# Kernel optimization log

Hardware: AMD Instinct MI355X
Metric: run time of the kernel (lower is better)

Reference implementation:

```python
import jax, jax.numpy as jnp
import numpy as np

NEG_INF = -1e30
LRELU_SLOPE = 0.01
KEEP_SCALE = 2.0  # 1/(1-p) with p=0.5


def mixed_act(x, tid):
    # x: [B, H], tid: [H] int type ids
    # 0 relu, 1 tanh, 2 sig, 3 'smin'->Softmax, 4 'smax'->Softmin, 5 gelu, 6 lrelu
    relu = jnp.maximum(x, 0.0)
    tanh = jnp.tanh(x)
    sig = jax.nn.sigmoid(x)
    gelu = jax.nn.gelu(x, approximate=False)
    lrelu = jnp.where(x >= 0, x, LRELU_SLOPE * x)
    # softmax/softmin restricted to the columns of that type (matches x[:, idx] gather)
    smin = jax.nn.softmax(jnp.where(tid == 3, x, NEG_INF), axis=1)
    smax = jax.nn.softmax(jnp.where(tid == 4, -x, NEG_INF), axis=1)
    return jnp.select(
        [tid == 0, tid == 1, tid == 2, tid == 3, tid == 4, tid == 5, tid == 6],
        [relu, tanh, sig, smin, smax, gelu, lrelu],
    )


def setup_inputs() -> dict:
    key = jax.random.key(0)
    ks = jax.random.split(key, 16)
    B, D_IN, H, C = 32768, 784, 1024, 10
    s_in, s_h = 1.0 / np.sqrt(D_IN), 1.0 / np.sqrt(H)
    inp = {
        "x": jax.random.normal(ks[0], (B, D_IN), jnp.float32),
        "W0": jax.random.normal(ks[1], (H, D_IN), jnp.float32) * s_in,
        "b0": jax.random.normal(ks[2], (H,), jnp.float32) * s_in,
        "W1": jax.random.normal(ks[3], (H, H), jnp.float32) * s_h,
        "b1": jax.random.normal(ks[4], (H,), jnp.float32) * s_h,
        "W2": jax.random.normal(ks[5], (H, H), jnp.float32) * s_h,
        "b2": jax.random.normal(ks[6], (H,), jnp.float32) * s_h,
        "W3": jax.random.normal(ks[7], (C, H), jnp.float32) * s_h,
        "b3": jax.random.normal(ks[8], (C,), jnp.float32) * s_h,
        "mask1": jax.random.bernoulli(ks[9], 0.5, (B, H)).astype(jnp.float32),
        "mask2": jax.random.bernoulli(ks[10], 0.5, (B, H)).astype(jnp.float32),
        "mask3": jax.random.bernoulli(ks[11], 0.5, (B, H)).astype(jnp.float32),
        "type_ids": jax.random.randint(ks[12], (3, H), 0, 7, jnp.int32),
    }
    return inp


def reference(x, W0, b0, W1, b1, W2, b2, W3, b3, mask1, mask2, mask3, type_ids):
    h = mixed_act(x @ W0.T + b0, type_ids[0])
    h = mixed_act((h * mask1 * KEEP_SCALE) @ W1.T + b1, type_ids[1])
    h = mixed_act((h * mask2 * KEEP_SCALE) @ W2.T + b2, type_ids[2])
    logits = (h * mask3 * KEEP_SCALE) @ W3.T + b3
    out = jax.nn.log_softmax(logits, axis=1)
    return (out, mask1, mask2, mask3)
```

## Files before the change

kernel.cpp:

```cpp
#include <hip/hip_runtime.h>
#include <hip/hip_bf16.h>
#include <cstdint>
#include <cstddef>

typedef __bf16 bf16_t;
typedef bf16_t bf16x8 __attribute__((ext_vector_type(8)));
typedef bf16_t bf16x4 __attribute__((ext_vector_type(4)));
typedef float f32x4 __attribute__((ext_vector_type(4)));

#define NEG_BIG (-1e30f)

__global__ __launch_bounds__(256) void convert_pad(const float* __restrict__ src,
                                                   bf16_t* __restrict__ dst,
                                                   int incols, int outcols) {
    const int row = blockIdx.x;
    const float* s = src + (size_t)row * incols;
    bf16_t* d = dst + (size_t)row * outcols;
    const int n4 = outcols >> 2;
    for (int c = threadIdx.x; c < n4; c += blockDim.x) {
        const int col = c << 2;
        float4 v;
        if (col < incols) v = *(const float4*)(s + col);
        else              v = make_float4(0.f, 0.f, 0.f, 0.f);
        bf16x4 o;
        o[0] = (bf16_t)v.x; o[1] = (bf16_t)v.y; o[2] = (bf16_t)v.z; o[3] = (bf16_t)v.w;
        *(bf16x4*)(d + col) = o;
    }
}

#define BM 128
#define BN 128
#define BK 32

__global__ __launch_bounds__(256) void gemm_bt(const bf16_t* __restrict__ A,
                                               const bf16_t* __restrict__ W,
                                               const float* __restrict__ bias,
                                               bf16_t* __restrict__ Z,
                                               int K, int N) {
    __shared__ __align__(16) bf16_t As[BM * BK];
    __shared__ __align__(16) bf16_t Bs[BN * BK];
    const int tid  = threadIdx.x;
    const int wid  = tid >> 6;
    const int lane = tid & 63;
    const int n0 = blockIdx.x * BN;
    const int m0 = blockIdx.y * BM;

    const int wm = (wid >> 1) * 64;
    const int wn = (wid & 1) * 64;

    f32x4 acc[4][4] = {};

    const int srow0 = wid * 32 + (lane >> 2);
    const int scol  = (lane & 3) * 8;

    const bf16_t* Aptr0 = A + (size_t)(m0 + srow0) * K + scol;
    const bf16_t* Aptr1 = A + (size_t)(m0 + srow0 + 16) * K + scol;
    const bf16_t* Wptr0 = W + (size_t)(n0 + srow0) * K + scol;
    const bf16_t* Wptr1 = W + (size_t)(n0 + srow0 + 16) * K + scol;

    bf16_t* AsB0 = As + (wid * 2 + 0) * 512;
    bf16_t* AsB1 = As + (wid * 2 + 1) * 512;
    bf16_t* BsB0 = Bs + (wid * 2 + 0) * 512;
    bf16_t* BsB1 = Bs + (wid * 2 + 1) * 512;

    for (int k0 = 0; k0 < K; k0 += BK) {
        __syncthreads();
        __builtin_amdgcn_global_load_lds((const __attribute__((address_space(1))) void*)(Aptr0 + k0),
                                         (__attribute__((address_space(3))) void*)AsB0, 16, 0, 0);
        __builtin_amdgcn_global_load_lds((const __attribute__((address_space(1))) void*)(Aptr1 + k0),
                                         (__attribute__((address_space(3))) void*)AsB1, 16, 0, 0);
        __builtin_amdgcn_global_load_lds((const __attribute__((address_space(1))) void*)(Wptr0 + k0),
                                         (__attribute__((address_space(3))) void*)BsB0, 16, 0, 0);
        __builtin_amdgcn_global_load_lds((const __attribute__((address_space(1))) void*)(Wptr1 + k0),
                                         (__attribute__((address_space(3))) void*)BsB1, 16, 0, 0);
        __syncthreads();

        const int arow = wm + (lane & 15);
        const int brow = wn + (lane & 15);
        const int koff = (lane >> 4) * 8;
        bf16x8 af[4], bfr[4];
        #pragma unroll
        for (int i = 0; i < 4; ++i)
            af[i] = *(const bf16x8*)(As + (arow + i * 16) * BK + koff);
        #pragma unroll
        for (int j = 0; j < 4; ++j)
            bfr[j] = *(const bf16x8*)(Bs + (brow + j * 16) * BK + koff);
        #pragma unroll
        for (int i = 0; i < 4; ++i)
            #pragma unroll
            for (int j = 0; j < 4; ++j)
                acc[i][j] = __builtin_amdgcn_mfma_f32_16x16x32_bf16(af[i], bfr[j], acc[i][j], 0, 0, 0);
    }

    const int cq = lane >> 4;
    const int cl = lane & 15;
    #pragma unroll
    for (int j = 0; j < 4; ++j) {
        const int col = n0 + wn + j * 16 + cl;
        const float bj = bias[col];
        #pragma unroll
        for (int i = 0; i < 4; ++i) {
            const int row = m0 + wm + i * 16 + cq * 4;
            #pragma unroll
            for (int r = 0; r < 4; ++r)
                Z[(size_t)(row + r) * N + col] = (bf16_t)(acc[i][j][r] + bj);
        }
    }
}

__device__ __forceinline__ float wave_max(float v) {
    #pragma unroll
    for (int off = 32; off > 0; off >>= 1) v = fmaxf(v, __shfl_xor(v, off));
    return v;
}
__device__ __forceinline__ float wave_sum(float v) {
    #pragma unroll
    for (int off = 32; off > 0; off >>= 1) v += __shfl_xor(v, off);
    return v;
}

__global__ __launch_bounds__(256) void act_kernel(const bf16_t* __restrict__ Z,
                                                  const float* __restrict__ mask,
                                                  const int* __restrict__ tids,
                                                  bf16_t* __restrict__ H,
                                                  float* __restrict__ mask_out) {
    const int wid  = threadIdx.x >> 6;
    const int lane = threadIdx.x & 63;
    const int row  = blockIdx.x * 4 + wid;
    const size_t rb = (size_t)row * 1024;

    float z[16], mk[16];
    int   ty[16];
    #pragma unroll
    for (int c = 0; c < 4; ++c) {
        const int col = c * 256 + lane * 4;
        const bf16x4 zv = *(const bf16x4*)(Z + rb + col);
        const float4 mv = *(const float4*)(mask + rb + col);
        const int4   tv = *(const int4*)(tids + col);
        z[c*4+0] = (float)zv[0]; z[c*4+1] = (float)zv[1];
        z[c*4+2] = (float)zv[2]; z[c*4+3] = (float)zv[3];
        mk[c*4+0] = mv.x; mk[c*4+1] = mv.y; mk[c*4+2] = mv.z; mk[c*4+3] = mv.w;
        ty[c*4+0] = tv.x; ty[c*4+1] = tv.y; ty[c*4+2] = tv.z; ty[c*4+3] = tv.w;
    }

    float mx3 = NEG_BIG, mx4 = NEG_BIG;
    #pragma unroll
    for (int j = 0; j < 16; ++j) {
        if (ty[j] == 3) mx3 = fmaxf(mx3, z[j]);
        if (ty[j] == 4) mx4 = fmaxf(mx4, -z[j]);
    }
    mx3 = wave_max(mx3);
    mx4 = wave_max(mx4);

    float s3 = 0.f, s4 = 0.f;
    #pragma unroll
    for (int j = 0; j < 16; ++j) {
        if (ty[j] == 3) s3 += __expf(z[j] - mx3);
        if (ty[j] == 4) s4 += __expf(-z[j] - mx4);
    }
    s3 = wave_sum(s3);
    s4 = wave_sum(s4);
    const float inv3 = 1.f / s3;
    const float inv4 = 1.f / s4;

    #pragma unroll
    for (int c = 0; c < 4; ++c) {
        const int col = c * 256 + lane * 4;
        bf16x4 h4;
        float4 m4;
        #pragma unroll
        for (int j = 0; j < 4; ++j) {
            const int k = c * 4 + j;
            const float zz = z[k];
            const int   tt = ty[k];
            float a;
            if (tt == 0)      a = fmaxf(zz, 0.f);
            else if (tt == 1) { const float e = __expf(-2.f * fabsf(zz));
                                const float th = (1.f - e) / (1.f + e);
                                a = (zz >= 0.f) ? th : -th; }
            else if (tt == 2) a = 1.f / (1.f + __expf(-zz));
            else if (tt == 3) a = __expf(zz - mx3) * inv3;
            else if (tt == 4) a = __expf(-zz - mx4) * inv4;
            else if (tt == 5) a = 0.5f * zz * (1.f + erff(zz * 0.70710678118654752f));
            else              a = (zz >= 0.f) ? zz : 0.01f * zz;
            h4[j] = (bf16_t)(a * mk[k] * 2.0f);
        }
        m4.x = mk[c*4+0]; m4.y = mk[c*4+1]; m4.z = mk[c*4+2]; m4.w = mk[c*4+3];
        *(bf16x4*)(H + rb + col) = h4;
        *(float4*)(mask_out + rb + col) = m4;
    }
}

__global__ __launch_bounds__(256) void final_layer(const bf16_t* __restrict__ H,
                                                   const float* __restrict__ W3,
                                                   const float* __restrict__ b3,
                                                   float* __restrict__ out) {
    __shared__ __align__(16) bf16_t Ws[10 * 1024];
    for (int i = threadIdx.x; i < 10240; i += 256) Ws[i] = (bf16_t)W3[i];
    __syncthreads();
    const int wid  = threadIdx.x >> 6;
    const int lane = threadIdx.x & 63;
    #pragma unroll 1
    for (int rr = 0; rr < 4; ++rr) {
        const int row = blockIdx.x * 16 + wid * 4 + rr;
        const bf16_t* hrow = H + (size_t)row * 1024;
        float acc[10];
        #pragma unroll
        for (int n = 0; n < 10; ++n) acc[n] = 0.f;
        #pragma unroll
        for (int c = 0; c < 2; ++c) {
            const int k = c * 512 + lane * 8;
            const bf16x8 hv = *(const bf16x8*)(hrow + k);
            float hf[8];
            #pragma unroll
            for (int j = 0; j < 8; ++j) hf[j] = (float)hv[j];
            #pragma unroll
            for (int n = 0; n < 10; ++n) {
                const bf16x8 wv = *(const bf16x8*)(Ws + n * 1024 + k);
                #pragma unroll
                for (int j = 0; j < 8; ++j) acc[n] += hf[j] * (float)wv[j];
            }
        }
        #pragma unroll
        for (int n = 0; n < 10; ++n)
            #pragma unroll
            for (int off = 32; off > 0; off >>= 1)
                acc[n] += __shfl_down(acc[n], off);
        if (lane == 0) {
            float lg[10]; float mx = -1e30f;
            #pragma unroll
            for (int n = 0; n < 10; ++n) { lg[n] = acc[n] + b3[n]; mx = fmaxf(mx, lg[n]); }
            float se = 0.f;
            #pragma unroll
            for (int n = 0; n < 10; ++n) se += __expf(lg[n] - mx);
            const float lse = logf(se) + mx;
            #pragma unroll
            for (int n = 0; n < 10; ++n) out[(size_t)row * 10 + n] = lg[n] - lse;
        }
    }
}

extern "C" void kernel_launch(void* const* d_in, const int* in_sizes, int n_in,
                              void* d_out, int out_size, void* d_ws, size_t ws_size,
                              hipStream_t stream) {
    (void)in_sizes; (void)n_in; (void)out_size; (void)ws_size;
    const float* x     = (const float*)d_in[0];
    const float* W0    = (const float*)d_in[1];
    const float* b0    = (const float*)d_in[2];
    const float* W1    = (const float*)d_in[3];
    const float* b1    = (const float*)d_in[4];
    const float* W2    = (const float*)d_in[5];
    const float* b2    = (const float*)d_in[6];
    const float* W3    = (const float*)d_in[7];
    const float* b3    = (const float*)d_in[8];
    const float* mask1 = (const float*)d_in[9];
    const float* mask2 = (const float*)d_in[10];
    const float* mask3 = (const float*)d_in[11];
    const int*   tids  = (const int*)d_in[12];

    float* out = (float*)d_out;
    float* mo1 = out + 327680;
    float* mo2 = mo1 + 33554432;
    float* mo3 = mo2 + 33554432;

    char* ws = (char*)d_ws;
    bf16_t* xb  = (bf16_t*)ws;  ws += (size_t)32768 * 800 * 2;
    bf16_t* W0b = (bf16_t*)ws;  ws += (size_t)1024 * 800 * 2;
    bf16_t* W1b = (bf16_t*)ws;  ws += (size_t)1024 * 1024 * 2;
    bf16_t* W2b = (bf16_t*)ws;  ws += (size_t)1024 * 1024 * 2;
    bf16_t* Zb  = (bf16_t*)ws;  ws += (size_t)32768 * 1024 * 2;
    bf16_t* hb  = (bf16_t*)ws;  ws += (size_t)32768 * 1024 * 2;

    convert_pad<<<32768, 256, 0, stream>>>(x,  xb,  784, 800);
    convert_pad<<<1024,  256, 0, stream>>>(W0, W0b, 784, 800);
    convert_pad<<<1024,  256, 0, stream>>>(W1, W1b, 1024, 1024);
    convert_pad<<<1024,  256, 0, stream>>>(W2, W2b, 1024, 1024);

    dim3 g(1024 / BN, 32768 / BM);
    gemm_bt<<<g, 256, 0, stream>>>(xb, W0b, b0, Zb, 800, 1024);
    act_kernel<<<8192, 256, 0, stream>>>(Zb, mask1, tids, hb, mo1);
    gemm_bt<<<g, 256, 0, stream>>>(hb, W1b, b1, Zb, 1024, 1024);
    act_kernel<<<8192, 256, 0, stream>>>(Zb, mask2, tids + 1024, hb, mo2);
    gemm_bt<<<g, 256, 0, stream>>>(hb, W2b, b2, Zb, 1024, 1024);
    act_kernel<<<8192, 256, 0, stream>>>(Zb, mask3, tids + 2048, hb, mo3);
    final_layer<<<2048, 256, 0, stream>>>(hb, W3, b3, out);
}
```

Before: 1.199 ms.

## Fuse all forward stages into one persistent cooperative kernel with grid syncs

Replaces the eleven separate kernel launches with a single persistent cooperative kernel. Each stage is a grid-stride loop over its tiles or rows, and stages are separated by grid.sync(). This removes launch overhead and inter-kernel gaps. In exchange the grid is limited to the number of co-resident blocks, so the GEMM tiles lose some scheduling flexibility, and grid barriers add their own cost. The original multi-kernel path is kept as a fallback if the cooperative launch fails.

```diff
diff --git a/kernel.cpp b/kernel.cpp
--- a/kernel.cpp
+++ b/kernel.cpp
@@ -1,7 +1,10 @@
 #include <hip/hip_runtime.h>
 #include <hip/hip_bf16.h>
+#include <hip/hip_cooperative_groups.h>
 #include <cstdint>
 #include <cstddef>
+
+namespace cg = cooperative_groups;
 
 typedef __bf16 bf16_t;
 typedef bf16_t bf16x8 __attribute__((ext_vector_type(8)));
@@ -9,15 +12,18 @@
 typedef float f32x4 __attribute__((ext_vector_type(4)));
 
 #define NEG_BIG (-1e30f)
-
-__global__ __launch_bounds__(256) void convert_pad(const float* __restrict__ src,
-                                                   bf16_t* __restrict__ dst,
-                                                   int incols, int outcols) {
-    const int row = blockIdx.x;
+#define BM 128
+#define BN 128
+#define BK 32
+
+
+__device__ __forceinline__ void convert_row(const float* __restrict__ src,
+                                            bf16_t* __restrict__ dst,
+                                            int incols, int outcols, int row) {
     const float* s = src + (size_t)row * incols;
     bf16_t* d = dst + (size_t)row * outcols;
     const int n4 = outcols >> 2;
-    for (int c = threadIdx.x; c < n4; c += blockDim.x) {
+    for (int c = threadIdx.x; c < n4; c += 256) {
         const int col = c << 2;
         float4 v;
         if (col < incols) v = *(const float4*)(s + col);
@@ -28,22 +34,19 @@
     }
 }
 
-#define BM 128
-#define BN 128
-#define BK 32
-
-__global__ __launch_bounds__(256) void gemm_bt(const bf16_t* __restrict__ A,
-                                               const bf16_t* __restrict__ W,
-                                               const float* __restrict__ bias,
-                                               bf16_t* __restrict__ Z,
-                                               int K, int N) {
-    __shared__ __align__(16) bf16_t As[BM * BK];
-    __shared__ __align__(16) bf16_t Bs[BN * BK];
+__device__ __forceinline__ void gemm_tile(char* smem,
+                                          const bf16_t* __restrict__ A,
+                                          const bf16_t* __restrict__ W,
+                                          const float* __restrict__ bias,
+                                          bf16_t* __restrict__ Z,
+                                          int K, int tile) {
+    bf16_t* As = (bf16_t*)smem;
+    bf16_t* Bs = (bf16_t*)(smem + 8192);
     const int tid  = threadIdx.x;
     const int wid  = tid >> 6;
     const int lane = tid & 63;
-    const int n0 = blockIdx.x * BN;
-    const int m0 = blockIdx.y * BM;
+    const int n0 = (tile & 7) * BN;
+    const int m0 = (tile >> 3) * BM;
 
     const int wm = (wid >> 1) * 64;
     const int wn = (wid & 1) * 64;
@@ -103,7 +106,7 @@
             const int row = m0 + wm + i * 16 + cq * 4;
             #pragma unroll
             for (int r = 0; r < 4; ++r)
-                Z[(size_t)(row + r) * N + col] = (bf16_t)(acc[i][j][r] + bj);
+                Z[(size_t)(row + r) * 1024 + col] = (bf16_t)(acc[i][j][r] + bj);
         }
     }
 }
@@ -119,14 +122,14 @@
     return v;
 }
 
-__global__ __launch_bounds__(256) void act_kernel(const bf16_t* __restrict__ Z,
-                                                  const float* __restrict__ mask,
-                                                  const int* __restrict__ tids,
-                                                  bf16_t* __restrict__ H,
-                                                  float* __restrict__ mask_out) {
+__device__ __forceinline__ void act_rows(const bf16_t* __restrict__ Z,
+                                         const float* __restrict__ mask,
+                                         const int* __restrict__ tids,
+                                         bf16_t* __restrict__ H,
+                                         float* __restrict__ mask_out, int rg) {
     const int wid  = threadIdx.x >> 6;
     const int lane = threadIdx.x & 63;
-    const int row  = blockIdx.x * 4 + wid;
+    const int row  = rg * 4 + wid;
     const size_t rb = (size_t)row * 1024;
 
     float z[16], mk[16];
@@ -191,6 +194,115 @@
     }
 }
 
+__device__ __forceinline__ void final_block(const bf16_t* __restrict__ Ws,
+                                            const bf16_t* __restrict__ H,
+                                            const float* __restrict__ b3,
+                                            float* __restrict__ out, int b) {
+    const int wid  = threadIdx.x >> 6;
+    const int lane = threadIdx.x & 63;
+    #pragma unroll 1
+    for (int rr = 0; rr < 4; ++rr) {
+        const int row = b * 16 + wid * 4 + rr;
+        const bf16_t* hrow = H + (size_t)row * 1024;
+        float acc[10];
+        #pragma unroll
+        for (int n = 0; n < 10; ++n) acc[n] = 0.f;
+        #pragma unroll
+        for (int c = 0; c < 2; ++c) {
+            const int k = c * 512 + lane * 8;
+            const bf16x8 hv = *(const bf16x8*)(hrow + k);
+            float hf[8];
+            #pragma unroll
+            for (int j = 0; j < 8; ++j) hf[j] = (float)hv[j];
+            #pragma unroll
+            for (int n = 0; n < 10; ++n) {
+                const bf16x8 wv = *(const bf16x8*)(Ws + n * 1024 + k);
+                #pragma unroll
+                for (int j = 0; j < 8; ++j) acc[n] += hf[j] * (float)wv[j];
+            }
+        }
+        #pragma unroll
+        for (int n = 0; n < 10; ++n)
+            #pragma unroll
+            for (int off = 32; off > 0; off >>= 1)
+                acc[n] += __shfl_down(acc[n], off);
+        if (lane == 0) {
+            float lg[10]; float mx = -1e30f;
+            #pragma unroll
+            for (int n = 0; n < 10; ++n) { lg[n] = acc[n] + b3[n]; mx = fmaxf(mx, lg[n]); }
+            float se = 0.f;
+            #pragma unroll
+            for (int n = 0; n < 10; ++n) se += __expf(lg[n] - mx);
+            const float lse = logf(se) + mx;
+            #pragma unroll
+            for (int n = 0; n < 10; ++n) out[(size_t)row * 10 + n] = lg[n] - lse;
+        }
+    }
+}
+
+
+struct FusedParams {
+    const float *x, *W0, *b0, *W1, *b1, *W2, *b2, *W3, *b3;
+    const float *mask1, *mask2, *mask3;
+    const int* tids;
+    bf16_t *xb, *W0b, *W1b, *W2b, *Zb, *hb;
+    float *out, *mo1, *mo2, *mo3;
+};
+
+__global__ __launch_bounds__(256) void fused_forward(FusedParams p) {
+    cg::grid_group grid = cg::this_grid();
+    __shared__ __align__(16) char smem[20480];
+    const int nb  = gridDim.x;
+    const int bid = blockIdx.x;
+
+    for (int r = bid; r < 32768; r += nb) convert_row(p.x,  p.xb,  784, 800, r);
+    for (int r = bid; r < 1024;  r += nb) convert_row(p.W0, p.W0b, 784, 800, r);
+    for (int r = bid; r < 1024;  r += nb) convert_row(p.W1, p.W1b, 1024, 1024, r);
+    for (int r = bid; r < 1024;  r += nb) convert_row(p.W2, p.W2b, 1024, 1024, r);
+    grid.sync();
+    for (int t = bid; t < 2048; t += nb) gemm_tile(smem, p.xb, p.W0b, p.b0, p.Zb, 800, t);
+    grid.sync();
+    for (int r = bid; r < 8192; r += nb) act_rows(p.Zb, p.mask1, p.tids, p.hb, p.mo1, r);
+    grid.sync();
+    for (int t = bid; t < 2048; t += nb) gemm_tile(smem, p.hb, p.W1b, p.b1, p.Zb, 1024, t);
+    grid.sync();
+    for (int r = bid; r < 8192; r += nb) act_rows(p.Zb, p.mask2, p.tids + 1024, p.hb, p.mo2, r);
+    grid.sync();
+    for (int t = bid; t < 2048; t += nb) gemm_tile(smem, p.hb, p.W2b, p.b2, p.Zb, 1024, t);
+    grid.sync();
+    for (int r = bid; r < 8192; r += nb) act_rows(p.Zb, p.mask3, p.tids + 2048, p.hb, p.mo3, r);
+    grid.sync();
+    {
+        bf16_t* Ws = (bf16_t*)smem;
+        for (int i = threadIdx.x; i < 10240; i += 256) Ws[i] = (bf16_t)p.W3[i];
+        __syncthreads();
+        for (int b = bid; b < 2048; b += nb) final_block(Ws, p.hb, p.b3, p.out, b);
+    }
+}
+
+
+__global__ __launch_bounds__(256) void convert_pad(const float* __restrict__ src,
+                                                   bf16_t* __restrict__ dst,
+                                                   int incols, int outcols) {
+    convert_row(src, dst, incols, outcols, blockIdx.x);
+}
+
+__global__ __launch_bounds__(256) void gemm_bt(const bf16_t* __restrict__ A,
+                                               const bf16_t* __restrict__ W,
+                                               const float* __restrict__ bias,
+                                               bf16_t* __restrict__ Z, int K) {
+    __shared__ __align__(16) char smem[16384];
+    gemm_tile(smem, A, W, bias, Z, K, blockIdx.y * 8 + blockIdx.x);
+}
+
+__global__ __launch_bounds__(256) void act_kernel(const bf16_t* __restrict__ Z,
+                                                  const float* __restrict__ mask,
+                                                  const int* __restrict__ tids,
+                                                  bf16_t* __restrict__ H,
+                                                  float* __restrict__ mask_out) {
+    act_rows(Z, mask, tids, H, mask_out, blockIdx.x);
+}
+
 __global__ __launch_bounds__(256) void final_layer(const bf16_t* __restrict__ H,
                                                    const float* __restrict__ W3,
                                                    const float* __restrict__ b3,
@@ -198,90 +310,70 @@
     __shared__ __align__(16) bf16_t Ws[10 * 1024];
     for (int i = threadIdx.x; i < 10240; i += 256) Ws[i] = (bf16_t)W3[i];
     __syncthreads();
-    const int wid  = threadIdx.x >> 6;
-    const int lane = threadIdx.x & 63;
-    #pragma unroll 1
-    for (int rr = 0; rr < 4; ++rr) {
-        const int row = blockIdx.x * 16 + wid * 4 + rr;
-        const bf16_t* hrow = H + (size_t)row * 1024;
-        float acc[10];
-        #pragma unroll
-        for (int n = 0; n < 10; ++n) acc[n] = 0.f;
-        #pragma unroll
-        for (int c = 0; c < 2; ++c) {
-            const int k = c * 512 + lane * 8;
-            const bf16x8 hv = *(const bf16x8*)(hrow + k);
-            float hf[8];
-            #pragma unroll
-            for (int j = 0; j < 8; ++j) hf[j] = (float)hv[j];
-            #pragma unroll
-            for (int n = 0; n < 10; ++n) {
-                const bf16x8 wv = *(const bf16x8*)(Ws + n * 1024 + k);
-                #pragma unroll
-                for (int j = 0; j < 8; ++j) acc[n] += hf[j] * (float)wv[j];
-            }
-        }
-        #pragma unroll
-        for (int n = 0; n < 10; ++n)
-            #pragma unroll
-            for (int off = 32; off > 0; off >>= 1)
-                acc[n] += __shfl_down(acc[n], off);
-        if (lane == 0) {
-            float lg[10]; float mx = -1e30f;
-            #pragma unroll
-            for (int n = 0; n < 10; ++n) { lg[n] = acc[n] + b3[n]; mx = fmaxf(mx, lg[n]); }
-            float se = 0.f;
-            #pragma unroll
-            for (int n = 0; n < 10; ++n) se += __expf(lg[n] - mx);
-            const float lse = logf(se) + mx;
-            #pragma unroll
-            for (int n = 0; n < 10; ++n) out[(size_t)row * 10 + n] = lg[n] - lse;
-        }
-    }
-}
+    final_block(Ws, H, b3, out, blockIdx.x);
+}
+
 
 extern "C" void kernel_launch(void* const* d_in, const int* in_sizes, int n_in,
                               void* d_out, int out_size, void* d_ws, size_t ws_size,
                               hipStream_t stream) {
     (void)in_sizes; (void)n_in; (void)out_size; (void)ws_size;
-    const float* x     = (const float*)d_in[0];
-    const float* W0    = (const float*)d_in[1];
-    const float* b0    = (const float*)d_in[2];
-    const float* W1    = (const float*)d_in[3];
-    const float* b1    = (const float*)d_in[4];
-    const float* W2    = (const float*)d_in[5];
-    const float* b2    = (const float*)d_in[6];
-    const float* W3    = (const float*)d_in[7];
-    const float* b3    = (const float*)d_in[8];
-    const float* mask1 = (const float*)d_in[9];
-    const float* mask2 = (const float*)d_in[10];
-    const float* mask3 = (const float*)d_in[11];
-    const int*   tids  = (const int*)d_in[12];
-
-    float* out = (float*)d_out;
-    float* mo1 = out + 327680;
-    float* mo2 = mo1 + 33554432;
-    float* mo3 = mo2 + 33554432;
+    FusedParams p;
+    p.x     = (const float*)d_in[0];
+    p.W0    = (const float*)d_in[1];
+    p.b0    = (const float*)d_in[2];
+    p.W1    = (const float*)d_in[3];
+    p.b1    = (const float*)d_in[4];
+    p.W2    = (const float*)d_in[5];
+    p.b2    = (const float*)d_in[6];
+    p.W3    = (const float*)d_in[7];
+    p.b3    = (const float*)d_in[8];
+    p.mask1 = (const float*)d_in[9];
+    p.mask2 = (const float*)d_in[10];
+    p.mask3 = (const float*)d_in[11];
+    p.tids  = (const int*)d_in[12];
+
+    p.out = (float*)d_out;
+    p.mo1 = p.out + 327680;
+    p.mo2 = p.mo1 + 33554432;
+    p.mo3 = p.mo2 + 33554432;
 
     char* ws = (char*)d_ws;
-    bf16_t* xb  = (bf16_t*)ws;  ws += (size_t)32768 * 800 * 2;
-    bf16_t* W0b = (bf16_t*)ws;  ws += (size_t)1024 * 800 * 2;
-    bf16_t* W1b = (bf16_t*)ws;  ws += (size_t)1024 * 1024 * 2;
-    bf16_t* W2b = (bf16_t*)ws;  ws += (size_t)1024 * 1024 * 2;
-    bf16_t* Zb  = (bf16_t*)ws;  ws += (size_t)32768 * 1024 * 2;
-    bf16_t* hb  = (bf16_t*)ws;  ws += (size_t)32768 * 1024 * 2;
-
-    convert_pad<<<32768, 256, 0, stream>>>(x,  xb,  784, 800);
-    convert_pad<<<1024,  256, 0, stream>>>(W0, W0b, 784, 800);
-    convert_pad<<<1024,  256, 0, stream>>>(W1, W1b, 1024, 1024);
-    convert_pad<<<1024,  256, 0, stream>>>(W2, W2b, 1024, 1024);
-
-    dim3 g(1024 / BN, 32768 / BM);
-    gemm_bt<<<g, 256, 0, stream>>>(xb, W0b, b0, Zb, 800, 1024);
-    act_kernel<<<8192, 256, 0, stream>>>(Zb, mask1, tids, hb, mo1);
-    gemm_bt<<<g, 256, 0, stream>>>(hb, W1b, b1, Zb, 1024, 1024);
-    act_kernel<<<8192, 256, 0, stream>>>(Zb, mask2, tids + 1024, hb, mo2);
-    gemm_bt<<<g, 256, 0, stream>>>(hb, W2b, b2, Zb, 1024, 1024);
-    act_kernel<<<8192, 256, 0, stream>>>(Zb, mask3, tids + 2048, hb, mo3);
-    final_layer<<<2048, 256, 0, stream>>>(hb, W3, b3, out);
-}
+    p.xb  = (bf16_t*)ws;  ws += (size_t)32768 * 800 * 2;
+    p.W0b = (bf16_t*)ws;  ws += (size_t)1024 * 800 * 2;
+    p.W1b = (bf16_t*)ws;  ws += (size_t)1024 * 1024 * 2;
+    p.W2b = (bf16_t*)ws;  ws += (size_t)1024 * 1024 * 2;
+    p.Zb  = (bf16_t*)ws;  ws += (size_t)32768 * 1024 * 2;
+    p.hb  = (bf16_t*)ws;  ws += (size_t)32768 * 1024 * 2;
+
+    int perCU = 0;
+    hipError_t oerr = hipOccupancyMaxActiveBlocksPerMultiprocessor(
+        &perCU, (const void*)fused_forward, 256, 0);
+    bool launched = false;
+    if (oerr == hipSuccess && perCU >= 1) {
+        int blocks = perCU * 256;
+        if (blocks > 2048) blocks = 2048;
+        void* kargs[] = { (void*)&p };
+        hipError_t lerr = hipLaunchCooperativeKernel(
+            (const void*)fused_forward, dim3(blocks), dim3(256), kargs, 0, stream);
+        if (lerr == hipSuccess) launched = true;
+        else (void)hipGetLastError();
+    } else {
+        (void)hipGetLastError();
+    }
+
+    if (!launched) {
+        convert_pad<<<32768, 256, 0, stream>>>(p.x,  p.xb,  784, 800);
+        convert_pad<<<1024,  256, 0, stream>>>(p.W0, p.W0b, 784, 800);
+        convert_pad<<<1024,  256, 0, stream>>>(p.W1, p.W1b, 1024, 1024);
+        convert_pad<<<1024,  256, 0, stream>>>(p.W2, p.W2b, 1024, 1024);
+        dim3 g(8, 256);
+        gemm_bt<<<g, 256, 0, stream>>>(p.xb, p.W0b, p.b0, p.Zb, 800);
+        act_kernel<<<8192, 256, 0, stream>>>(p.Zb, p.mask1, p.tids, p.hb, p.mo1);
+        gemm_bt<<<g, 256, 0, stream>>>(p.hb, p.W1b, p.b1, p.Zb, 1024);
+        act_kernel<<<8192, 256, 0, stream>>>(p.Zb, p.mask2, p.tids + 1024, p.hb, p.mo2);
+        gemm_bt<<<g, 256, 0, stream>>>(p.hb, p.W2b, p.b2, p.Zb, 1024);
+        act_kernel<<<8192, 256, 0, stream>>>(p.Zb, p.mask3, p.tids + 2048, p.hb, p.mo3);
+        final_layer<<<2048, 256, 0, stream>>>(p.hb, p.W3, p.b3, p.out);
+    }
+}
```

Measured after the change: 1.193 ms. No clear change (-0.5%).
